# Performance work log

Hardware: AMD Instinct MI355X
Metric: run time of the kernel (lower is better)

The kernel has to match this reference:

```python
import jax, jax.numpy as jnp
import numpy as np

NUM_CLUSTERS = 128
C = NUM_CLUSTERS + 1  # bincount minlength = number_clusters + 1
SOFTMAX_TEMP = 1.0


def setup_inputs() -> dict:
    key = jax.random.key(0)
    k1, k2, k3, k4 = jax.random.split(key, 4)
    B, N, D = 32, 4096, 64
    Bc = 4  # clusters batch dim; heads = B // Bc = 8
    return {
        "queries": jax.random.normal(k1, (B, N, D), dtype=jnp.float32),
        "keys": jax.random.normal(k2, (B, N, D), dtype=jnp.float32),
        "values": jax.random.normal(k3, (B, N, D), dtype=jnp.float32),
        "clusters": jax.random.randint(k4, (Bc, N), 0, C).astype(jnp.int64),
    }


def _segment_sum_batched(x, groups, num_segments):
    # x: [B, N, D], groups: [B, N] -> [B, num_segments, D]
    return jax.vmap(lambda xb, gb: jax.ops.segment_sum(xb, gb, num_segments=num_segments))(x, groups)


def reference(queries, keys, values, clusters):
    B, N, D = queries.shape
    Bc = clusters.shape[0]
    rep = B // Bc
    g = clusters.astype(jnp.int32)
    # per-cluster counts (bincount with minlength=C)
    counts = jax.vmap(lambda gb: jax.ops.segment_sum(jnp.ones((N,), jnp.float32), gb, num_segments=C))(g)
    # repeat assignments/counts across heads: torch .repeat(rep, 1) == tile on dim 0
    groups = jnp.tile(g, (rep, 1))          # [B, N]
    counts = jnp.tile(counts, (rep, 1))     # [B, C]
    w = jnp.where(counts > 0, 1.0 / counts, 0.0)  # 1/counts (guard empty clusters)

    Q_center = _segment_sum_batched(queries, groups, C) * w[..., None]  # [B, C, D]
    K_center = _segment_sum_batched(keys, groups, C) * w[..., None]
    V_center = _segment_sum_batched(values, groups, C) * w[..., None]

    QK = jnp.einsum('bqd,bkd->bqk', Q_center, K_center)  # [B, C, C]
    A = jax.nn.softmax(SOFTMAX_TEMP * QK, axis=-1)
    # weighted softmax: reweight by key-cluster counts, renormalize
    A = A * counts[:, None, :]
    A_full = A / A.sum(axis=-1, keepdims=True)

    V = jnp.einsum('bqk,bkd->bqd', A_full, V_center)  # [B, C, D]
    # Broadcast centers back to all cluster members (gather)
    out = jnp.take_along_axis(V, groups[..., None], axis=1)  # [B, N, D]
    return out, A_full[:, :, 0]
```

## Files before the change

kernel.cpp:

```cpp
#include <hip/hip_runtime.h>

#define B_ 32
#define N_ 4096
#define D_ 64
#define C_ 129
#define BC_ 4
#define CG_ 33
#define QROWS_ 17

__global__ __launch_bounds__(1024) void k_sort(const int* __restrict__ cl,
                                               float* __restrict__ counts,
                                               int* __restrict__ offsets,
                                               int* __restrict__ sidx) {
    __shared__ int cnt[C_];
    __shared__ int base[C_];
    __shared__ int cur[C_];
    int bc = blockIdx.x, tid = threadIdx.x;
    for (int i = tid; i < C_; i += 1024) { cnt[i] = 0; cur[i] = 0; }
    __syncthreads();
    const int4* g4 = (const int4*)(cl + bc * N_);
    for (int n = tid; n < N_ / 4; n += 1024) {
        int4 c4 = g4[n];
        atomicAdd(&cnt[c4.x], 1);
        atomicAdd(&cnt[c4.y], 1);
        atomicAdd(&cnt[c4.z], 1);
        atomicAdd(&cnt[c4.w], 1);
    }
    __syncthreads();
    if (tid < C_) {
        int acc = 0;
        for (int i = 0; i < tid; i++) acc += cnt[i];
        base[tid] = acc;
    }
    __syncthreads();
    for (int i = tid; i < C_; i += 1024) {
        counts[bc * C_ + i] = (float)cnt[i];
        offsets[bc * (C_ + 1) + i] = base[i];
    }
    if (tid == 0) offsets[bc * (C_ + 1) + C_] = N_;
    for (int n = tid; n < N_ / 4; n += 1024) {
        int4 c4 = g4[n];
        int n0 = n * 4;
        sidx[bc * N_ + base[c4.x] + atomicAdd(&cur[c4.x], 1)] = n0;
        sidx[bc * N_ + base[c4.y] + atomicAdd(&cur[c4.y], 1)] = n0 + 1;
        sidx[bc * N_ + base[c4.z] + atomicAdd(&cur[c4.z], 1)] = n0 + 2;
        sidx[bc * N_ + base[c4.w] + atomicAdd(&cur[c4.w], 1)] = n0 + 3;
    }
}

__global__ __launch_bounds__(256) void k_segsum4(const float* __restrict__ q,
                                                 const float* __restrict__ k,
                                                 const float* __restrict__ v,
                                                 const int* __restrict__ offsets,
                                                 const int* __restrict__ sidx,
                                                 float* __restrict__ sums) {
    int bid = blockIdx.x;
    int cg = bid % CG_;
    int b = bid / CG_;
    int wave = threadIdx.x >> 6, lane = threadIdx.x & 63;
    int c = cg * 4 + wave;
    if (c >= C_) return;
    int bc = b & 3;
    int start = offsets[bc * (C_ + 1) + c];
    int end = offsets[bc * (C_ + 1) + c + 1];
    int cnt = end - start;
    int sub = lane >> 4, d4 = lane & 15;

    const float4* q4 = (const float4*)(q + (size_t)b * N_ * D_);
    const float4* k4 = (const float4*)(k + (size_t)b * N_ * D_);
    const float4* v4 = (const float4*)(v + (size_t)b * N_ * D_);
    const int* si = sidx + bc * N_;

    float4 aq = make_float4(0.f, 0.f, 0.f, 0.f);
    float4 ak = make_float4(0.f, 0.f, 0.f, 0.f);
    float4 av = make_float4(0.f, 0.f, 0.f, 0.f);

    if (cnt > 0) {
        int last = end - 1;
        int ia = start + sub, ib = ia + 4, ic = ia + 8, id = ia + 12;
        int ra = si[min(ia, last)], rb = si[min(ib, last)];
        int rc = si[min(ic, last)], rd = si[min(id, last)];
        for (int i0 = start; i0 < end; i0 += 16) {
            int ca = ia, cb = ib, cc = ic, cd = id;
            int ua = ra, ub = rb, uc = rc, ud = rd;
            ia += 16; ib += 16; ic += 16; id += 16;
            if (i0 + 16 < end) {
                ra = si[min(ia, last)]; rb = si[min(ib, last)];
                rc = si[min(ic, last)]; rd = si[min(id, last)];
            }
            float ma = (ca < end) ? 1.f : 0.f;
            float mb = (cb < end) ? 1.f : 0.f;
            float mc = (cc < end) ? 1.f : 0.f;
            float md = (cd < end) ? 1.f : 0.f;
            float4 qa = q4[ua * 16 + d4], qb = q4[ub * 16 + d4];
            float4 qc = q4[uc * 16 + d4], qd = q4[ud * 16 + d4];
            float4 ka = k4[ua * 16 + d4], kb = k4[ub * 16 + d4];
            float4 kc = k4[uc * 16 + d4], kd = k4[ud * 16 + d4];
            float4 va = v4[ua * 16 + d4], vb = v4[ub * 16 + d4];
            float4 vc = v4[uc * 16 + d4], vd = v4[ud * 16 + d4];
            aq.x += ma * qa.x + mb * qb.x + mc * qc.x + md * qd.x;
            aq.y += ma * qa.y + mb * qb.y + mc * qc.y + md * qd.y;
            aq.z += ma * qa.z + mb * qb.z + mc * qc.z + md * qd.z;
            aq.w += ma * qa.w + mb * qb.w + mc * qc.w + md * qd.w;
            ak.x += ma * ka.x + mb * kb.x + mc * kc.x + md * kd.x;
            ak.y += ma * ka.y + mb * kb.y + mc * kc.y + md * kd.y;
            ak.z += ma * ka.z + mb * kb.z + mc * kc.z + md * kd.z;
            ak.w += ma * ka.w + mb * kb.w + mc * kc.w + md * kd.w;
            av.x += ma * va.x + mb * vb.x + mc * vc.x + md * vd.x;
            av.y += ma * va.y + mb * vb.y + mc * vc.y + md * vd.y;
            av.z += ma * va.z + mb * vb.z + mc * vc.z + md * vd.z;
            av.w += ma * va.w + mb * vb.w + mc * vc.w + md * vd.w;
        }
    }
#pragma unroll
    for (int off = 16; off <= 32; off <<= 1) {
        aq.x += __shfl_xor(aq.x, off, 64); aq.y += __shfl_xor(aq.y, off, 64);
        aq.z += __shfl_xor(aq.z, off, 64); aq.w += __shfl_xor(aq.w, off, 64);
        ak.x += __shfl_xor(ak.x, off, 64); ak.y += __shfl_xor(ak.y, off, 64);
        ak.z += __shfl_xor(ak.z, off, 64); ak.w += __shfl_xor(ak.w, off, 64);
        av.x += __shfl_xor(av.x, off, 64); av.y += __shfl_xor(av.y, off, 64);
        av.z += __shfl_xor(av.z, off, 64); av.w += __shfl_xor(av.w, off, 64);
    }
    if (sub == 0) {
        float w = (cnt > 0) ? 1.f / (float)cnt : 0.f;
        float4 oq = make_float4(aq.x * w, aq.y * w, aq.z * w, aq.w * w);
        float4 ok = make_float4(ak.x * w, ak.y * w, ak.z * w, ak.w * w);
        float4 ov = make_float4(av.x * w, av.y * w, av.z * w, av.w * w);
        ((float4*)(sums + (size_t)b * C_ * D_))[c * 16 + d4] = oq;
        ((float4*)(sums + ((size_t)B_ + b) * C_ * D_))[c * 16 + d4] = ok;
        ((float4*)(sums + ((size_t)2 * B_ + b) * C_ * D_))[c * 16 + d4] = ov;
    }
}

__global__ __launch_bounds__(256, 2) void k_attn_sc(const float* __restrict__ sums,
                                                    const float* __restrict__ counts,
                                                    const int* __restrict__ offsets,
                                                    const int* __restrict__ sidx,
                                                    float* __restrict__ out,
                                                    float* __restrict__ aout) {
    __shared__ float4 kc4[C_ * 17];
    __shared__ float4 vc4[C_ * 17];
    __shared__ float cnt_s[C_];
    __shared__ float arow[4][4][132];

    int b = blockIdx.x >> 3;
    int qg = blockIdx.x & 7;
    int q0 = qg * QROWS_;
    int qcnt = min(QROWS_, C_ - q0);
    int tid = threadIdx.x;
    int bc = b & 3;

    for (int i = tid; i < C_; i += 256)
        cnt_s[i] = counts[bc * C_ + i];

    const float4* qsum4 = (const float4*)(sums + (size_t)b * C_ * D_);
    const float4* ksum4 = (const float4*)(sums + ((size_t)B_ + b) * C_ * D_);
    const float4* vsum4 = (const float4*)(sums + ((size_t)2 * B_ + b) * C_ * D_);

    for (int i = tid; i < C_ * 16; i += 256) {
        int c = i >> 4, d4 = i & 15;
        kc4[c * 17 + d4] = ksum4[i];
        vc4[c * 17 + d4] = vsum4[i];
    }
    __syncthreads();

    const int* si = sidx + bc * N_;
    float4* ob = (float4*)(out + (size_t)b * N_ * D_);

    int wave = __builtin_amdgcn_readfirstlane(tid >> 6);
    int lane = tid & 63;

    for (int tt = wave; tt * 4 < qcnt; tt += 4) {
        int t4 = tt * 4;
        const float4* qp0 = qsum4 + (size_t)(q0 + min(t4 + 0, qcnt - 1)) * 16;
        const float4* qp1 = qsum4 + (size_t)(q0 + min(t4 + 1, qcnt - 1)) * 16;
        const float4* qp2 = qsum4 + (size_t)(q0 + min(t4 + 2, qcnt - 1)) * 16;
        const float4* qp3 = qsum4 + (size_t)(q0 + min(t4 + 3, qcnt - 1)) * 16;
        float s0[4] = {0, 0, 0, 0}, s1[4] = {0, 0, 0, 0}, s2[4] = {0, 0, 0, 0};
#pragma unroll 4
        for (int d4 = 0; d4 < 16; d4++) {
            float4 kv0 = kc4[lane * 17 + d4];
            float4 kv1 = kc4[(lane + 64) * 17 + d4];
            float4 kv2 = kc4[128 * 17 + d4];
            float4 qv0 = qp0[d4], qv1 = qp1[d4], qv2 = qp2[d4], qv3 = qp3[d4];
            s0[0] += qv0.x * kv0.x + qv0.y * kv0.y + qv0.z * kv0.z + qv0.w * kv0.w;
            s1[0] += qv0.x * kv1.x + qv0.y * kv1.y + qv0.z * kv1.z + qv0.w * kv1.w;
            s2[0] += qv0.x * kv2.x + qv0.y * kv2.y + qv0.z * kv2.z + qv0.w * kv2.w;
            s0[1] += qv1.x * kv0.x + qv1.y * kv0.y + qv1.z * kv0.z + qv1.w * kv0.w;
            s1[1] += qv1.x * kv1.x + qv1.y * kv1.y + qv1.z * kv1.z + qv1.w * kv1.w;
            s2[1] += qv1.x * kv2.x + qv1.y * kv2.y + qv1.z * kv2.z + qv1.w * kv2.w;
            s0[2] += qv2.x * kv0.x + qv2.y * kv0.y + qv2.z * kv0.z + qv2.w * kv0.w;
            s1[2] += qv2.x * kv1.x + qv2.y * kv1.y + qv2.z * kv1.z + qv2.w * kv1.w;
            s2[2] += qv2.x * kv2.x + qv2.y * kv2.y + qv2.z * kv2.z + qv2.w * kv2.w;
            s0[3] += qv3.x * kv0.x + qv3.y * kv0.y + qv3.z * kv0.z + qv3.w * kv0.w;
            s1[3] += qv3.x * kv1.x + qv3.y * kv1.y + qv3.z * kv1.z + qv3.w * kv1.w;
            s2[3] += qv3.x * kv2.x + qv3.y * kv2.y + qv3.z * kv2.z + qv3.w * kv2.w;
        }
#pragma unroll
        for (int r = 0; r < 4; r++) {
            if (t4 + r >= qcnt) break;
            int qrow = q0 + t4 + r;
            float m = fmaxf(s0[r], s1[r]);
            if (lane == 0) m = fmaxf(m, s2[r]);
            for (int off = 32; off > 0; off >>= 1)
                m = fmaxf(m, __shfl_xor(m, off, 64));
            float e0 = __expf(s0[r] - m) * cnt_s[lane];
            float e1 = __expf(s1[r] - m) * cnt_s[lane + 64];
            float e2 = (lane == 0) ? __expf(s2[r] - m) * cnt_s[128] : 0.f;
            float sum = e0 + e1 + e2;
            for (int off = 32; off > 0; off >>= 1)
                sum += __shfl_xor(sum, off, 64);
            float inv = 1.f / sum;
            float a0 = e0 * inv, a1 = e1 * inv;
            arow[wave][r][lane] = a0;
            arow[wave][r][64 + lane] = a1;
            if (lane == 0) {
                arow[wave][r][128] = e2 * inv;
                aout[b * C_ + qrow] = a0;
            }
        }
        __builtin_amdgcn_s_waitcnt(0);
        __builtin_amdgcn_sched_barrier(0);
        int rr = lane >> 4, d4 = lane & 15;
        const float4* ar4 = (const float4*)arow[wave][rr];
        float4 o = make_float4(0.f, 0.f, 0.f, 0.f);
        for (int k4 = 0; k4 < 32; k4++) {
            float4 a4 = ar4[k4];
            float4 v0 = vc4[(k4 * 4 + 0) * 17 + d4];
            float4 v1 = vc4[(k4 * 4 + 1) * 17 + d4];
            float4 v2 = vc4[(k4 * 4 + 2) * 17 + d4];
            float4 v3 = vc4[(k4 * 4 + 3) * 17 + d4];
            o.x += a4.x * v0.x + a4.y * v1.x + a4.z * v2.x + a4.w * v3.x;
            o.y += a4.x * v0.y + a4.y * v1.y + a4.z * v2.y + a4.w * v3.y;
            o.z += a4.x * v0.z + a4.y * v1.z + a4.z * v2.z + a4.w * v3.z;
            o.w += a4.x * v0.w + a4.y * v1.w + a4.z * v2.w + a4.w * v3.w;
        }
        {
            float a128 = arow[wave][rr][128];
            float4 vv = vc4[128 * 17 + d4];
            o.x += a128 * vv.x; o.y += a128 * vv.y;
            o.z += a128 * vv.z; o.w += a128 * vv.w;
        }
        if (t4 + rr < qcnt) {
            int qrow = q0 + t4 + rr;
            int s = offsets[bc * (C_ + 1) + qrow];
            int e = offsets[bc * (C_ + 1) + qrow + 1];
            for (int mm = s; mm < e; mm++) {
                int n = si[mm];
                ob[n * 16 + d4] = o;
            }
        }
    }
}

extern "C" void kernel_launch(void* const* d_in, const int* in_sizes, int n_in,
                              void* d_out, int out_size, void* d_ws, size_t ws_size,
                              hipStream_t stream) {
    const float* q = (const float*)d_in[0];
    const float* k = (const float*)d_in[1];
    const float* v = (const float*)d_in[2];
    const int* cl = (const int*)d_in[3];
    float* out = (float*)d_out;
    float* aout = out + (size_t)B_ * N_ * D_;

    float* ws = (float*)d_ws;
    float* counts = ws;
    float* sums = ws + 1024;
    int* offsets = (int*)(sums + (size_t)3 * B_ * C_ * D_);
    int* sidx = offsets + 4 * (C_ + 1);

    k_sort<<<BC_, 1024, 0, stream>>>(cl, counts, offsets, sidx);
    k_segsum4<<<B_ * CG_, 256, 0, stream>>>(q, k, v, offsets, sidx, sums);
    k_attn_sc<<<B_ * 8, 256, 0, stream>>>(sums, counts, offsets, sidx, out, aout);
}
```

Baseline: 171.0 us.

## Split attention rows across more blocks and halve per-wave row batch

Reduces query rows per block from 17 to 8 and launches 17*B blocks instead of 8*B, with batch index as the fast-varying block index. Each wave now handles 2 query rows instead of 4, splitting the AV reduction across two half-waves with a shuffle combine and interleaving the scatter of output rows between halves. This is meant to raise parallelism for the scatter-bound output write, at the cost of reloading K/V centers into shared memory in more blocks.

```diff
diff --git a/kernel.cpp b/kernel.cpp
--- a/kernel.cpp
+++ b/kernel.cpp
@@ -6,7 +6,7 @@
 #define C_ 129
 #define BC_ 4
 #define CG_ 33
-#define QROWS_ 17
+#define QROWS_ 8
 
 __global__ __launch_bounds__(1024) void k_sort(const int* __restrict__ cl,
                                                float* __restrict__ counts,
@@ -141,10 +141,11 @@
     __shared__ float4 kc4[C_ * 17];
     __shared__ float4 vc4[C_ * 17];
     __shared__ float cnt_s[C_];
-    __shared__ float arow[4][4][132];
-
-    int b = blockIdx.x >> 3;
-    int qg = blockIdx.x & 7;
+    __shared__ float arow[4][2][132];
+
+    int bid = blockIdx.x;
+    int b = bid & 31;
+    int qg = bid >> 5;
     int q0 = qg * QROWS_;
     int qcnt = min(QROWS_, C_ - q0);
     int tid = threadIdx.x;
@@ -170,36 +171,28 @@
     int wave = __builtin_amdgcn_readfirstlane(tid >> 6);
     int lane = tid & 63;
 
-    for (int tt = wave; tt * 4 < qcnt; tt += 4) {
-        int t4 = tt * 4;
-        const float4* qp0 = qsum4 + (size_t)(q0 + min(t4 + 0, qcnt - 1)) * 16;
-        const float4* qp1 = qsum4 + (size_t)(q0 + min(t4 + 1, qcnt - 1)) * 16;
-        const float4* qp2 = qsum4 + (size_t)(q0 + min(t4 + 2, qcnt - 1)) * 16;
-        const float4* qp3 = qsum4 + (size_t)(q0 + min(t4 + 3, qcnt - 1)) * 16;
-        float s0[4] = {0, 0, 0, 0}, s1[4] = {0, 0, 0, 0}, s2[4] = {0, 0, 0, 0};
+    for (int tt = wave; tt * 2 < qcnt; tt += 4) {
+        int t2 = tt * 2;
+        const float4* qp0 = qsum4 + (size_t)(q0 + min(t2 + 0, qcnt - 1)) * 16;
+        const float4* qp1 = qsum4 + (size_t)(q0 + min(t2 + 1, qcnt - 1)) * 16;
+        float s0[2] = {0, 0}, s1[2] = {0, 0}, s2[2] = {0, 0};
 #pragma unroll 4
         for (int d4 = 0; d4 < 16; d4++) {
             float4 kv0 = kc4[lane * 17 + d4];
             float4 kv1 = kc4[(lane + 64) * 17 + d4];
             float4 kv2 = kc4[128 * 17 + d4];
-            float4 qv0 = qp0[d4], qv1 = qp1[d4], qv2 = qp2[d4], qv3 = qp3[d4];
+            float4 qv0 = qp0[d4], qv1 = qp1[d4];
             s0[0] += qv0.x * kv0.x + qv0.y * kv0.y + qv0.z * kv0.z + qv0.w * kv0.w;
             s1[0] += qv0.x * kv1.x + qv0.y * kv1.y + qv0.z * kv1.z + qv0.w * kv1.w;
             s2[0] += qv0.x * kv2.x + qv0.y * kv2.y + qv0.z * kv2.z + qv0.w * kv2.w;
             s0[1] += qv1.x * kv0.x + qv1.y * kv0.y + qv1.z * kv0.z + qv1.w * kv0.w;
             s1[1] += qv1.x * kv1.x + qv1.y * kv1.y + qv1.z * kv1.z + qv1.w * kv1.w;
             s2[1] += qv1.x * kv2.x + qv1.y * kv2.y + qv1.z * kv2.z + qv1.w * kv2.w;
-            s0[2] += qv2.x * kv0.x + qv2.y * kv0.y + qv2.z * kv0.z + qv2.w * kv0.w;
-            s1[2] += qv2.x * kv1.x + qv2.y * kv1.y + qv2.z * kv1.z + qv2.w * kv1.w;
-            s2[2] += qv2.x * kv2.x + qv2.y * kv2.y + qv2.z * kv2.z + qv2.w * kv2.w;
-            s0[3] += qv3.x * kv0.x + qv3.y * kv0.y + qv3.z * kv0.z + qv3.w * kv0.w;
-            s1[3] += qv3.x * kv1.x + qv3.y * kv1.y + qv3.z * kv1.z + qv3.w * kv1.w;
-            s2[3] += qv3.x * kv2.x + qv3.y * kv2.y + qv3.z * kv2.z + qv3.w * kv2.w;
         }
 #pragma unroll
-        for (int r = 0; r < 4; r++) {
-            if (t4 + r >= qcnt) break;
-            int qrow = q0 + t4 + r;
+        for (int r = 0; r < 2; r++) {
+            if (t2 + r >= qcnt) break;
+            int qrow = q0 + t2 + r;
             float m = fmaxf(s0[r], s1[r]);
             if (lane == 0) m = fmaxf(m, s2[r]);
             for (int off = 32; off > 0; off >>= 1)
@@ -221,10 +214,13 @@
         }
         __builtin_amdgcn_s_waitcnt(0);
         __builtin_amdgcn_sched_barrier(0);
-        int rr = lane >> 4, d4 = lane & 15;
+        int rr = lane >> 5;
+        int half = (lane >> 4) & 1;
+        int d4 = lane & 15;
         const float4* ar4 = (const float4*)arow[wave][rr];
         float4 o = make_float4(0.f, 0.f, 0.f, 0.f);
-        for (int k4 = 0; k4 < 32; k4++) {
+        int k4base = half * 16;
+        for (int k4 = k4base; k4 < k4base + 16; k4++) {
             float4 a4 = ar4[k4];
             float4 v0 = vc4[(k4 * 4 + 0) * 17 + d4];
             float4 v1 = vc4[(k4 * 4 + 1) * 17 + d4];
@@ -235,17 +231,21 @@
             o.z += a4.x * v0.z + a4.y * v1.z + a4.z * v2.z + a4.w * v3.z;
             o.w += a4.x * v0.w + a4.y * v1.w + a4.z * v2.w + a4.w * v3.w;
         }
+        o.x += __shfl_xor(o.x, 16, 64);
+        o.y += __shfl_xor(o.y, 16, 64);
+        o.z += __shfl_xor(o.z, 16, 64);
+        o.w += __shfl_xor(o.w, 16, 64);
         {
             float a128 = arow[wave][rr][128];
             float4 vv = vc4[128 * 17 + d4];
             o.x += a128 * vv.x; o.y += a128 * vv.y;
             o.z += a128 * vv.z; o.w += a128 * vv.w;
         }
-        if (t4 + rr < qcnt) {
-            int qrow = q0 + t4 + rr;
+        if (t2 + rr < qcnt) {
+            int qrow = q0 + t2 + rr;
             int s = offsets[bc * (C_ + 1) + qrow];
             int e = offsets[bc * (C_ + 1) + qrow + 1];
-            for (int mm = s; mm < e; mm++) {
+            for (int mm = s + half; mm < e; mm += 2) {
                 int n = si[mm];
                 ob[n * 16 + d4] = o;
             }
@@ -271,5 +271,5 @@
 
     k_sort<<<BC_, 1024, 0, stream>>>(cl, counts, offsets, sidx);
     k_segsum4<<<B_ * CG_, 256, 0, stream>>>(q, k, v, offsets, sidx, sums);
-    k_attn_sc<<<B_ * 8, 256, 0, stream>>>(sums, counts, offsets, sidx, out, aout);
-}
+    k_attn_sc<<<17 * B_, 256, 0, stream>>>(sums, counts, offsets, sidx, out, aout);
+}
```

Measured after the change: 164.7 us. -3.7%, faster.
